# Kernel optimization log

Measured on AMD Instinct MI355X. Metric: run time of the kernel, lower is better.

Reference implementation:

```python
import jax, jax.numpy as jnp
import numpy as np

B, C, H, W = 2, 64, 128, 128
K, SCALE, NUM_RES = 3, 2, 2
KK = K * K


def conv(x, w, b, pad=0):
    y = jax.lax.conv_general_dilated(x, w, (1, 1), [(pad, pad), (pad, pad)],
                                     dimension_numbers=('NCHW', 'OIHW', 'NCHW'))
    return y + b[None, :, None, None]


def unfold_dilated(x, k, d):
    # mimics nn.Unfold(kernel_size=k, dilation=d, padding=(k//2)*d) -> (b, c, k*k, h, w)
    pad = (k // 2) * d
    b, c, h, w = x.shape
    xp = jnp.pad(x, ((0, 0), (0, 0), (pad, pad), (pad, pad)))
    slices = [xp[:, :, i * d:i * d + h, j * d:j * d + w]
              for i in range(k) for j in range(k)]
    return jnp.stack(slices, axis=2)


def setup_inputs() -> dict:
    key = jax.random.key(0)
    ks = jax.random.split(key, 32)
    def p(k, shape, s=0.05):
        return jax.random.normal(k, shape, dtype=jnp.float32) * s
    H2, W2 = H * SCALE, W * SCALE
    return {
        'depth':  p(ks[0], (B, C, H2, W2), 1.0),
        'guide':  p(ks[1], (B, C, H2, W2), 1.0),
        'inputs': p(ks[2], (B, C, H, W), 1.0),
        # depth_kernel branch: 1x1 C->C (ReLU), 1x1 C->k^2
        'dk_w1': p(ks[3], (C, C, 1, 1)), 'dk_b1': jnp.zeros((C,), jnp.float32),
        'dk_w2': p(ks[4], (KK, C, 1, 1)), 'dk_b2': jnp.zeros((KK,), jnp.float32),
        # guide_kernel branch
        'gk_w1': p(ks[5], (C, C, 1, 1)), 'gk_b1': jnp.zeros((C,), jnp.float32),
        'gk_w2': p(ks[6], (KK, C, 1, 1)), 'gk_b2': jnp.zeros((KK,), jnp.float32),
        # weight_net: 3x3 2C->C (ReLU), 3x3 C->C (ReLU, TUnet stand-in), 3x3 C->1
        'wn_w1': p(ks[7], (C, 2 * C, 3, 3)), 'wn_b1': jnp.zeros((C,), jnp.float32),
        'wn_w2': p(ks[8], (C, C, 3, 3)), 'wn_b2': jnp.zeros((C,), jnp.float32),
        'wn_w3': p(ks[9], (1, C, 3, 3)), 'wn_b3': jnp.zeros((1,), jnp.float32),
        # residual blocks on inputs: NUM_RES x (conv3x3-ReLU-conv3x3 + skip)
        'rb_w': p(ks[10], (NUM_RES, 2, C, C, 3, 3)),
        'rb_b': jnp.zeros((NUM_RES, 2, C), jnp.float32),
        'aff_scale': 0.5 * KK * jnp.ones((1,), jnp.float32),
    }


def reference(depth, guide, inputs,
              dk_w1, dk_b1, dk_w2, dk_b2,
              gk_w1, gk_b1, gk_w2, gk_b2,
              wn_w1, wn_b1, wn_w2, wn_b2, wn_w3, wn_b3,
              rb_w, rb_b, aff_scale):
    # weight map
    wm = jax.nn.relu(conv(jnp.concatenate([depth, guide], axis=1), wn_w1, wn_b1, 1))
    wm = jax.nn.relu(conv(wm, wn_w2, wn_b2, 1))
    weight_map = conv(wm, wn_w3, wn_b3, 1)                       # (b,1,h_,w_)
    # per-pixel kernels
    dk = conv(jax.nn.relu(conv(depth, dk_w1, dk_b1)), dk_w2, dk_b2)
    gk = conv(jax.nn.relu(conv(guide, gk_w1, gk_b1)), gk_w2, gk_b2)
    dk = jax.nn.softmax(dk, axis=1)
    gk = jax.nn.softmax(gk, axis=1)
    fuse = weight_map * dk + (1.0 - weight_map) * gk
    fuse = jnp.tanh(fuse) / (aff_scale + 1e-8)
    ksum = jnp.maximum(jnp.sum(jnp.abs(fuse), axis=1, keepdims=True) + 1e-4, 1.0)
    fuse = fuse / ksum                                            # (b,k^2,h_,w_)
    # residual conv stack on low-res inputs
    x = inputs
    for i in range(NUM_RES):
        r = jax.nn.relu(conv(x, rb_w[i, 0], rb_b[i, 0], 1))
        r = conv(r, rb_w[i, 1], rb_b[i, 1], 1)
        x = x + r
    b, c, h, w = x.shape
    up = jax.image.resize(x, (b, c, h * SCALE, w * SCALE), method='bilinear')
    unf = unfold_dilated(up, K, SCALE)                            # (b,c,k^2,h_,w_)
    out = jnp.einsum('bkhw,bckhw->bchw', fuse, unf)
    return out
```

## Files before the change

kernel.cpp:

```cpp
#include <hip/hip_runtime.h>
#include <hip/hip_bf16.h>
#include <math.h>
#include <stdint.h>

#define HW2 (256*256)
#define HW1 (128*128)

typedef __attribute__((ext_vector_type(8))) short short8;
typedef __attribute__((ext_vector_type(4))) float floatx4;

__device__ __forceinline__ float b2f(ushort u) {
    union { unsigned int i; float f; } v; v.i = ((unsigned int)u) << 16; return v.f;
}
__device__ __forceinline__ ushort f2b(float f) {
    __hip_bfloat16 h = __float2bfloat16(f); return *(ushort*)&h;
}
__device__ __forceinline__ float fast_tanh(float x) {
    float cx = fminf(fmaxf(x, -15.f), 15.f);
    float t = __expf(2.f * cx);
    return (t - 1.f) / (t + 1.f);
}
__device__ __forceinline__ void gload_lds16(const void* g, void* l) {
    __builtin_amdgcn_global_load_lds(
        (__attribute__((address_space(1))) void*)(uintptr_t)g,
        (__attribute__((address_space(3))) void*)(unsigned)(uintptr_t)l,
        16, 0, 0);
}

__global__ __launch_bounds__(256)
void repack_all(const float* __restrict__ wn_w1, const float* __restrict__ wn_w2,
                const float* __restrict__ rb_w,
                const float* __restrict__ dk_w1, const float* __restrict__ gk_w1,
                const float* __restrict__ dk_w2, const float* __restrict__ gk_w2,
                const float* __restrict__ wn_w3,
                ushort* __restrict__ wt_wn1, ushort* __restrict__ wt_wn2,
                ushort* __restrict__ wt_rb,
                ushort* __restrict__ w1d, ushort* __restrict__ w1g,
                ushort* __restrict__ w2d, ushort* __restrict__ w2g,
                ushort* __restrict__ wt3) {
    int idx = blockIdx.x * 256 + threadIdx.x;
    int role = blockIdx.y;
    if (role == 0) {
        if (idx >= 73728) return;
        int o = idx / 1152; int rem = idx - o * 1152;
        int ci = rem / 9;   int t = rem - ci * 9;
        wt_wn1[(((size_t)(ci >> 5) * 9 + t) * 64 + o) * 32 + (ci & 31)] = f2b(wn_w1[idx]);
    } else if (role <= 5) {
        if (idx >= 36864) return;
        const float* w = (role == 1) ? wn_w2 : rb_w + (size_t)(role - 2) * 36864;
        ushort* wt     = (role == 1) ? wt_wn2 : wt_rb + (size_t)(role - 2) * 36864;
        int o = idx / 576; int rem = idx - o * 576;
        int ci = rem / 9;  int t = rem - ci * 9;
        wt[(((size_t)(ci >> 5) * 9 + t) * 64 + o) * 32 + (ci & 31)] = f2b(w[idx]);
    } else if (role == 6) {
        if (idx >= 10240) return;
        if (idx < 4096)      w1d[idx] = f2b(dk_w1[idx]);
        else if (idx < 8192) w1g[idx - 4096] = f2b(gk_w1[idx - 4096]);
        else if (idx < 9216) { int i = idx - 8192; w2d[i] = (i >> 6) < 9 ? f2b(dk_w2[i]) : (ushort)0; }
        else                 { int i = idx - 9216; w2g[i] = (i >> 6) < 9 ? f2b(gk_w2[i]) : (ushort)0; }
    } else {
        if (idx >= 9216) return;
        int kc = idx / 512; int rem = idx - kc * 512;
        int n = rem >> 5, c = rem & 31;
        int cc = kc / 9, t = kc - cc * 9;
        wt3[idx] = (n == 0) ? f2b(wn_w3[(cc * 32 + c) * 9 + t]) : (ushort)0;
    }
}

__global__ __launch_bounds__(256)
void to_chunked(const float* __restrict__ in, ushort* __restrict__ outc,
                int H, int W, int Cchunks) {
    int P = W + 2, Q = H + 2;
    int plane_px = P * Q;
    int idx = blockIdx.x * 256 + threadIdx.x;
    if (idx >= plane_px) return;
    int py = idx / P, px = idx - py * P;
    int bc = blockIdx.y;
    int b = bc / Cchunks, cc = bc - b * Cchunks;
    ushort* dst = outc + ((size_t)bc * plane_px + idx) * 32;
    short8* d8 = (short8*)dst;
    if (py == 0 || py == Q - 1 || px == 0 || px == P - 1) {
        short8 z = (short8){0, 0, 0, 0, 0, 0, 0, 0};
        d8[0] = z; d8[1] = z; d8[2] = z; d8[3] = z;
        return;
    }
    int y = py - 1, x = px - 1;
    const float* src = in + ((size_t)b * (Cchunks * 32) + cc * 32) * H * W
                          + (size_t)y * W + x;
    ushort tmp[32];
#pragma unroll
    for (int c = 0; c < 32; ++c)
        tmp[c] = f2b(src[(size_t)c * H * W]);
#pragma unroll
    for (int v = 0; v < 4; ++v) d8[v] = *(short8*)&tmp[v * 8];
}

__global__ __launch_bounds__(256)
void to_chunked_hi4(const float* __restrict__ depth, const float* __restrict__ guide,
                    ushort* __restrict__ outc) {
    int gid = blockIdx.x * 256 + threadIdx.x;
    int g   = gid & 63;
    int y   = (gid >> 6) & 255;
    int pl  = gid >> 14;
    const float* srcb = (pl < 4) ? depth : guide;
    int bc = pl & 3;
    int b = bc >> 1, cc = bc & 1;
    const float* src = srcb + ((size_t)b * 64 + cc * 32) * HW2 + (size_t)y * 256 + g * 4;
    ushort tmp[4][32];
#pragma unroll
    for (int c = 0; c < 32; ++c) {
        floatx4 v = *(const floatx4*)&src[(size_t)c * HW2];
        tmp[0][c] = f2b(v[0]); tmp[1][c] = f2b(v[1]);
        tmp[2][c] = f2b(v[2]); tmp[3][c] = f2b(v[3]);
    }
    ushort* dst = outc + ((size_t)pl * 258 * 258 + (size_t)(y + 1) * 258 + (g * 4 + 1)) * 32;
#pragma unroll
    for (int p = 0; p < 4; ++p) {
        short8* d8 = (short8*)(dst + (size_t)p * 32);
        d8[0] = *(short8*)&tmp[p][0];
        d8[1] = *(short8*)&tmp[p][8];
        d8[2] = *(short8*)&tmp[p][16];
        d8[3] = *(short8*)&tmp[p][24];
    }
}

__global__ __launch_bounds__(256)
void zero_border3(ushort* __restrict__ buf256, ushort* __restrict__ buf128,
                  ushort* __restrict__ bufhi) {
    int region = blockIdx.y;
    int H = (region == 1) ? 128 : 256;
    int P = H + 2, Q = H + 2;
    ushort* buf = (region == 0) ? buf256 : (region == 1) ? buf128 : bufhi;
    int nb = 2 * P + 2 * H;
    int idx = blockIdx.x * 256 + threadIdx.x;
    if (idx >= nb * 8) return;
    int pl = idx / nb, r = idx - pl * nb;
    int py, px;
    if (r < P)          { py = 0;     px = r; }
    else if (r < 2 * P) { py = Q - 1; px = r - P; }
    else { int k = r - 2 * P; py = 1 + (k >> 1); px = (k & 1) ? P - 1 : 0; }
    ushort* dst = buf + ((size_t)pl * P * Q + (size_t)py * P + px) * 32;
    short8 z = (short8){0, 0, 0, 0, 0, 0, 0, 0};
    short8* d8 = (short8*)dst;
    d8[0] = z; d8[1] = z; d8[2] = z; d8[3] = z;
}

template<int NCHUNK, int ROWS, bool RELU, bool HAS_SKIP, bool CONCAT2>
__global__ __launch_bounds__(256, 2)
void conv3x3_reg(const ushort* __restrict__ inA, const ushort* __restrict__ inB,
                 const ushort* __restrict__ wt, const float* __restrict__ bias,
                 const ushort* __restrict__ skip, ushort* __restrict__ outc,
                 int H, int W) {
    const int P = W + 2;
    const size_t plane = (size_t)P * (H + 2) * 32;
    int tid = threadIdx.x;
    int wv = tid >> 6, lane = tid & 63, ml = lane & 15, q = lane >> 4;
    int x0 = blockIdx.x * 16;
    int rowsPerBlock = (blockDim.x >> 6) * ROWS;
    int yb = blockIdx.y * rowsPerBlock + wv * ROWS;
    int b = blockIdx.z;

    floatx4 acc[ROWS][4];
#pragma unroll
    for (int r = 0; r < ROWS; ++r)
#pragma unroll
        for (int n = 0; n < 4; ++n) acc[r][n] = (floatx4){0.f, 0.f, 0.f, 0.f};

    for (int cc = 0; cc < NCHUNK; ++cc) {
        const ushort* base;
        if (CONCAT2) {
            constexpr int HC = NCHUNK / 2;
            if (cc < HC) base = inA + ((size_t)(b * HC + cc)) * plane;
            else         base = inB + ((size_t)(b * HC + cc - HC)) * plane;
        } else {
            base = inA + ((size_t)(b * NCHUNK + cc)) * plane;
        }
        const ushort* wb = wt + (size_t)cc * 18432;
#pragma unroll
        for (int dy = 0; dy < 3; ++dy) {
            short8 afr[3][ROWS], bfr[3][4];
#pragma unroll
            for (int dx = 0; dx < 3; ++dx) {
#pragma unroll
                for (int r = 0; r < ROWS; ++r)
                    afr[dx][r] = *(const short8*)&base[((size_t)(yb + r + dy) * P
                                                       + (x0 + ml + dx)) * 32 + q * 8];
#pragma unroll
                for (int n = 0; n < 4; ++n)
                    bfr[dx][n] = *(const short8*)&wb[(size_t)((dy * 3 + dx) * 64
                                                              + n * 16 + ml) * 32 + q * 8];
            }
#pragma unroll
            for (int dx = 0; dx < 3; ++dx)
#pragma unroll
                for (int r = 0; r < ROWS; ++r)
#pragma unroll
                    for (int n = 0; n < 4; ++n)
                        acc[r][n] = __builtin_amdgcn_mfma_f32_16x16x32_bf16(
                            afr[dx][r], bfr[dx][n], acc[r][n], 0, 0, 0);
        }
    }

#pragma unroll
    for (int r = 0; r < ROWS; ++r) {
        int y = yb + r;
#pragma unroll
        for (int n = 0; n < 4; ++n) {
            int ch = n * 16 + ml;
            int occ = ch >> 5, ocl = ch & 31;
            float bs = bias[ch];
            size_t pbase = ((size_t)(b * 2 + occ)) * plane + ((size_t)(y + 1) * P) * 32 + ocl;
#pragma unroll
            for (int e = 0; e < 4; ++e) {
                int x = x0 + q * 4 + e;
                float v = acc[r][n][e] + bs;
                if (RELU) v = fmaxf(v, 0.f);
                if (HAS_SKIP)
                    v += b2f(skip[((size_t)(b * 2 + occ)) * plane
                                  + ((size_t)(y + 1) * P + (x + 1)) * 32 + ocl]);
                outc[pbase + (size_t)(x + 1) * 32] = f2b(v);
            }
        }
    }
}

__global__ __launch_bounds__(256, 2)
void kernels_fuse_mfma(const ushort* __restrict__ depth_c, const ushort* __restrict__ guide_c,
                       const ushort* __restrict__ bufB,
                       const ushort* __restrict__ wt3, const float* __restrict__ wn_b3,
                       const ushort* __restrict__ w1d, const float* __restrict__ b1d,
                       const ushort* __restrict__ w2d, const float* __restrict__ b2d,
                       const ushort* __restrict__ w1g, const float* __restrict__ b1g,
                       const ushort* __restrict__ w2g, const float* __restrict__ b2g,
                       const float* __restrict__ aff, float* __restrict__ fuse_out) {
    __shared__ __align__(16) ushort stage[12672];
    __shared__ __align__(16) ushort hid[2][4][16 * 72];
    __shared__ float wmv[4][16];

    int tid = threadIdx.x;
    int wv = tid >> 6, lane = tid & 63, ml = lane & 15, q = lane >> 4;
    int p0 = blockIdx.x * 64 + wv * 16;
    int b = p0 >> 16, rem0 = p0 & 65535;
    const size_t plane = (size_t)258 * 258 * 32;

    int rem = rem0 + ml;
    int y = rem >> 8, x = rem & 255;
    size_t poff = ((size_t)(y + 1) * 258 + (x + 1)) * 32;

    int pb  = blockIdx.x * 64;
    int y0  = (pb & 65535) >> 8;
    int x0b = pb & 255;

    short8 afr[2][2];
#pragma unroll
    for (int kc = 0; kc < 2; ++kc) {
        afr[0][kc] = *(const short8*)&depth_c[(size_t)(b * 2 + kc) * plane + poff + q * 8];
        afr[1][kc] = *(const short8*)&guide_c[(size_t)(b * 2 + kc) * plane + poff + q * 8];
    }

    const ushort* bbase = bufB + (size_t)(b * 2) * plane;
#pragma unroll
    for (int i = 0; i < 7; ++i) {
        int wofs = i * 4096 + (wv << 10);
        int ofs  = wofs + (lane << 4);
        if (ofs < 25344) {
            int seg = ofs / 4224;
            int within = ofs - seg * 4224;
            int cc2 = seg / 3, r = seg - cc2 * 3;
            const ushort* gsrc = bbase + (size_t)cc2 * plane
                               + ((size_t)(y0 + r) * 258 + x0b) * 32 + (within >> 1);
            gload_lds16(gsrc, (char*)stage + wofs);
        }
    }
    __syncthreads();

    floatx4 acc[2][4];
#pragma unroll
    for (int br = 0; br < 2; ++br)
#pragma unroll
        for (int nt = 0; nt < 4; ++nt) acc[br][nt] = (floatx4){0.f, 0.f, 0.f, 0.f};
#pragma unroll
    for (int nt = 0; nt < 4; ++nt)
#pragma unroll
        for (int kc = 0; kc < 2; ++kc) {
            short8 bD = *(const short8*)&w1d[(size_t)((nt * 16 + ml) * 64 + kc * 32 + q * 8)];
            short8 bG = *(const short8*)&w1g[(size_t)((nt * 16 + ml) * 64 + kc * 32 + q * 8)];
            acc[0][nt] = __builtin_amdgcn_mfma_f32_16x16x32_bf16(afr[0][kc], bD, acc[0][nt], 0, 0, 0);
            acc[1][nt] = __builtin_amdgcn_mfma_f32_16x16x32_bf16(afr[1][kc], bG, acc[1][nt], 0, 0, 0);
        }

    int colb = (wv << 4) + ml;
    floatx4 dw[4];
#pragma unroll
    for (int u = 0; u < 4; ++u) dw[u] = (floatx4){0.f, 0.f, 0.f, 0.f};
#pragma unroll
    for (int t = 0; t < 9; ++t) {
        int dy2 = t / 3, dx2 = t - 3 * dy2;
        short8 a0 = *(const short8*)&stage[(size_t)(dy2 * 66 + colb + dx2) * 32 + q * 8];
        short8 b3 = *(const short8*)&wt3[(size_t)(t * 512 + ml * 32 + q * 8)];
        dw[t & 3] = __builtin_amdgcn_mfma_f32_16x16x32_bf16(a0, b3, dw[t & 3], 0, 0, 0);
    }
#pragma unroll
    for (int t = 0; t < 9; ++t) {
        int dy2 = t / 3, dx2 = t - 3 * dy2;
        short8 a1 = *(const short8*)&stage[(size_t)((3 + dy2) * 66 + colb + dx2) * 32 + q * 8];
        short8 b3 = *(const short8*)&wt3[(size_t)((9 + t) * 512 + ml * 32 + q * 8)];
        dw[t & 3] = __builtin_amdgcn_mfma_f32_16x16x32_bf16(a1, b3, dw[t & 3], 0, 0, 0);
    }
    floatx4 dwm = (dw[0] + dw[1]) + (dw[2] + dw[3]);
    if (ml == 0) {
#pragma unroll
        for (int e = 0; e < 4; ++e) wmv[wv][q * 4 + e] = dwm[e];
    }

#pragma unroll
    for (int br = 0; br < 2; ++br) {
        const float* b1 = br ? b1g : b1d;
        ushort* h = hid[br][wv];
#pragma unroll
        for (int nt = 0; nt < 4; ++nt) {
            float bs = b1[nt * 16 + ml];
#pragma unroll
            for (int e = 0; e < 4; ++e) {
                float v = acc[br][nt][e] + bs;
                v = fmaxf(v, 0.f);
                h[(q * 4 + e) * 72 + nt * 16 + ml] = f2b(v);
            }
        }
    }

    floatx4 d2[2];
    d2[0] = (floatx4){0.f, 0.f, 0.f, 0.f};
    d2[1] = (floatx4){0.f, 0.f, 0.f, 0.f};
#pragma unroll
    for (int kc = 0; kc < 2; ++kc) {
        short8 a2d = *(const short8*)&w2d[(size_t)(ml * 64 + kc * 32 + q * 8)];
        short8 a2g = *(const short8*)&w2g[(size_t)(ml * 64 + kc * 32 + q * 8)];
        short8 hfd = *(const short8*)&hid[0][wv][ml * 72 + kc * 32 + q * 8];
        short8 hfg = *(const short8*)&hid[1][wv][ml * 72 + kc * 32 + q * 8];
        d2[0] = __builtin_amdgcn_mfma_f32_16x16x32_bf16(a2d, hfd, d2[0], 0, 0, 0);
        d2[1] = __builtin_amdgcn_mfma_f32_16x16x32_bf16(a2g, hfg, d2[1], 0, 0, 0);
    }

    float wm = wmv[wv][ml] + wn_b3[0];

    float sm[2][4];
#pragma unroll
    for (int br = 0; br < 2; ++br) {
        const float* b2 = br ? b2g : b2d;
        float lg[4];
#pragma unroll
        for (int e = 0; e < 4; ++e) {
            int j = q * 4 + e;
            lg[e] = (j < 9) ? (d2[br][e] + b2[j]) : -1e30f;
        }
        float m = fmaxf(fmaxf(lg[0], lg[1]), fmaxf(lg[2], lg[3]));
        m = fmaxf(m, __shfl_xor(m, 16));
        m = fmaxf(m, __shfl_xor(m, 32));
        float s = 0.f;
#pragma unroll
        for (int e = 0; e < 4; ++e) { lg[e] = __expf(lg[e] - m); s += lg[e]; }
        s += __shfl_xor(s, 16);
        s += __shfl_xor(s, 32);
        float inv = 1.f / s;
#pragma unroll
        for (int e = 0; e < 4; ++e) sm[br][e] = lg[e] * inv;
    }

    float inv_av = 1.f / (aff[0] + 1e-8f);
    float f[4];
    float s = 0.f;
#pragma unroll
    for (int e = 0; e < 4; ++e) {
        float v = wm * sm[0][e] + (1.f - wm) * sm[1][e];
        v = fast_tanh(v) * inv_av;
        f[e] = v;
        s += fabsf(v);
    }
    s += __shfl_xor(s, 16);
    s += __shfl_xor(s, 32);
    float ksum = s + 1e-4f;
    if (ksum < 1.f) ksum = 1.f;
    float invk = 1.f / ksum;
#pragma unroll
    for (int e = 0; e < 4; ++e) {
        int j = q * 4 + e;
        if (j < 9)
            fuse_out[((size_t)b * 9 + j) * HW2 + rem0 + ml] = f[e] * invk;
    }
}

__global__ __launch_bounds__(256)
void fuse_apply_up(const float* __restrict__ fuse, const ushort* __restrict__ r2c,
                   float* __restrict__ out) {
    int p = blockIdx.x * 256 + threadIdx.x;
    int pl = blockIdx.y;
    int b = pl >> 1, cc = pl & 1;
    int y = p >> 8, x = p & 255;

    int my = y >> 1, mx = x >> 1;
    float wyA = (y & 1) ? 0.75f : 0.25f;  float wyB = 1.f - wyA;
    float wxA = (x & 1) ? 0.75f : 0.25f;  float wxB = 1.f - wxA;
    int R0y = my + ((y & 1) ? 0 : -1) - 1;
    int R0x = mx + ((x & 1) ? 0 : -1) - 1;

    const float* f = fuse + (size_t)b * 9 * HW2 + p;
    float coef[4][4];
#pragma unroll
    for (int k = 0; k < 4; ++k)
#pragma unroll
        for (int l = 0; l < 4; ++l) coef[k][l] = 0.f;

#pragma unroll
    for (int ty = 0; ty < 3; ++ty) {
        int yp = y + (ty - 1) * 2;
        if (yp < 0 || yp > 255) continue;
#pragma unroll
        for (int tx = 0; tx < 3; ++tx) {
            int xp = x + (tx - 1) * 2;
            if (xp < 0 || xp > 255) continue;
            float fv = f[(size_t)(ty * 3 + tx) * HW2];
            coef[ty][tx]         += fv * wyA * wxA;
            coef[ty][tx + 1]     += fv * wyA * wxB;
            coef[ty + 1][tx]     += fv * wyB * wxA;
            coef[ty + 1][tx + 1] += fv * wyB * wxB;
        }
    }

    const ushort* base = r2c + (size_t)pl * 130 * 130 * 32;
    float acc[32];
#pragma unroll
    for (int c = 0; c < 32; ++c) acc[c] = 0.f;
#pragma unroll
    for (int k = 0; k < 4; ++k) {
        int ry = R0y + k; ry = ry < 0 ? 0 : (ry > 127 ? 127 : ry);
#pragma unroll
        for (int l = 0; l < 4; ++l) {
            int rx = R0x + l; rx = rx < 0 ? 0 : (rx > 127 ? 127 : rx);
            float cf = coef[k][l];
            const ushort* u = base + ((size_t)(ry + 1) * 130 + (rx + 1)) * 32;
#pragma unroll
            for (int c = 0; c < 32; ++c) acc[c] = fmaf(cf, b2f(u[c]), acc[c]);
        }
    }
    float* ob = out + ((size_t)(b * 64 + cc * 32)) * HW2 + p;
#pragma unroll
    for (int c = 0; c < 32; ++c) ob[(size_t)c * HW2] = acc[c];
}

extern "C" void kernel_launch(void* const* d_in, const int* in_sizes, int n_in,
                              void* d_out, int out_size, void* d_ws, size_t ws_size,
                              hipStream_t stream) {
    const float* depth  = (const float*)d_in[0];
    const float* guide  = (const float*)d_in[1];
    const float* inputs = (const float*)d_in[2];
    const float* dk_w1  = (const float*)d_in[3];
    const float* dk_b1  = (const float*)d_in[4];
    const float* dk_w2  = (const float*)d_in[5];
    const float* dk_b2  = (const float*)d_in[6];
    const float* gk_w1  = (const float*)d_in[7];
    const float* gk_b1  = (const float*)d_in[8];
    const float* gk_w2  = (const float*)d_in[9];
    const float* gk_b2  = (const float*)d_in[10];
    const float* wn_w1  = (const float*)d_in[11];
    const float* wn_b1  = (const float*)d_in[12];
    const float* wn_w2  = (const float*)d_in[13];
    const float* wn_b2  = (const float*)d_in[14];
    const float* wn_w3  = (const float*)d_in[15];
    const float* wn_b3  = (const float*)d_in[16];
    const float* rb_w   = (const float*)d_in[17];
    const float* rb_b   = (const float*)d_in[18];
    const float* aff    = (const float*)d_in[19];
    float* out = (float*)d_out;

    float* ws = (float*)d_ws;
    size_t off = 0;
    const size_t CH256 = 4260096;
    const size_t CH128 = 1081600;
    ushort* depth_c = (ushort*)(ws + off); off += CH256;
    ushort* guide_c = (ushort*)(ws + off); off += CH256;
    ushort* bufA    = (ushort*)(ws + off); off += CH256;
    ushort* bufB    = (ushort*)(ws + off); off += CH256;
    ushort* inp_c   = (ushort*)(ws + off); off += CH128;
    ushort* r0      = (ushort*)(ws + off); off += CH128;
    ushort* r1      = (ushort*)(ws + off); off += CH128;
    ushort* r2      = (ushort*)(ws + off); off += CH128;
    float* fuse     = ws + off; off += 1179648;
    ushort* wt_wn1  = (ushort*)(ws + off); off += 36864;
    ushort* wt_wn2  = (ushort*)(ws + off); off += 18432;
    ushort* wt_rb   = (ushort*)(ws + off); off += 73728;
    ushort* w1d_b   = (ushort*)(ws + off); off += 2048;
    ushort* w1g_b   = (ushort*)(ws + off); off += 2048;
    ushort* w2d_b   = (ushort*)(ws + off); off += 512;
    ushort* w2g_b   = (ushort*)(ws + off); off += 512;
    ushort* wt3_b   = (ushort*)(ws + off); off += 4608;

    repack_all<<<dim3(288, 8), 256, 0, stream>>>(
        wn_w1, wn_w2, rb_w, dk_w1, gk_w1, dk_w2, gk_w2, wn_w3,
        wt_wn1, wt_wn2, wt_rb, w1d_b, w1g_b, w2d_b, w2g_b, wt3_b);

    to_chunked_hi4<<<512, 256, 0, stream>>>(depth, guide, depth_c);
    to_chunked<<<dim3(67, 4), 256, 0, stream>>>(inputs, inp_c, 128, 128, 2);

    zero_border3<<<dim3(33, 3), 256, 0, stream>>>(bufA, r0, depth_c);

    conv3x3_reg<4, 4, true, false, true ><<<dim3(16, 16, 2), 256, 0, stream>>>(
        depth_c, guide_c, wt_wn1, wn_b1, nullptr, bufA, 256, 256);
    conv3x3_reg<2, 4, true, false, false><<<dim3(16, 16, 2), 256, 0, stream>>>(
        bufA, nullptr, wt_wn2, wn_b2, nullptr, bufB, 256, 256);

    kernels_fuse_mfma<<<2048, 256, 0, stream>>>(depth_c, guide_c, bufB,
                                                wt3_b, wn_b3,
                                                w1d_b, dk_b1, w2d_b, dk_b2,
                                                w1g_b, gk_b1, w2g_b, gk_b2,
                                                aff, fuse);

    conv3x3_reg<2, 2, true,  false, false><<<dim3(8, 16, 2), 256, 0, stream>>>(
        inp_c, nullptr, wt_rb + 0 * 36864, rb_b + 0 * 64, nullptr, r0, 128, 128);
    conv3x3_reg<2, 2, false, true,  false><<<dim3(8, 16, 2), 256, 0, stream>>>(
        r0, nullptr, wt_rb + 1 * 36864, rb_b + 1 * 64, inp_c, r1, 128, 128);
    conv3x3_reg<2, 2, true,  false, false><<<dim3(8, 16, 2), 256, 0, stream>>>(
        r1, nullptr, wt_rb + 2 * 36864, rb_b + 2 * 64, nullptr, r0, 128, 128);
    conv3x3_reg<2, 2, false, true,  false><<<dim3(8, 16, 2), 256, 0, stream>>>(
        r0, nullptr, wt_rb + 3 * 36864, rb_b + 3 * 64, r1, r2, 128, 128);

    fuse_apply_up<<<dim3(256, 4), 256, 0, stream>>>(fuse, r2, out);
}
```

Before: 327.9 us.

## Merge independent branch kernels into combined launches to cut launch count

The four preprocessing kernels are folded into one prep launch that dispatches on block index. The low-resolution residual conv stages are co-scheduled inside the same launches as the high-resolution weight-net convs and the fuse kernel, using extra grid slices. This cuts kernel launches from eleven to six and lets the small 128x128 convs fill idle compute units alongside the larger work. In exchange, the fused kernels share one launch-bounds/register configuration, and blocks of uneven cost run in the same grid.

```diff
diff --git a/kernel.cpp b/kernel.cpp
--- a/kernel.cpp
+++ b/kernel.cpp
@@ -27,19 +27,20 @@
         16, 0, 0);
 }
 
-__global__ __launch_bounds__(256)
-void repack_all(const float* __restrict__ wn_w1, const float* __restrict__ wn_w2,
-                const float* __restrict__ rb_w,
-                const float* __restrict__ dk_w1, const float* __restrict__ gk_w1,
-                const float* __restrict__ dk_w2, const float* __restrict__ gk_w2,
-                const float* __restrict__ wn_w3,
-                ushort* __restrict__ wt_wn1, ushort* __restrict__ wt_wn2,
-                ushort* __restrict__ wt_rb,
-                ushort* __restrict__ w1d, ushort* __restrict__ w1g,
-                ushort* __restrict__ w2d, ushort* __restrict__ w2g,
-                ushort* __restrict__ wt3) {
-    int idx = blockIdx.x * 256 + threadIdx.x;
-    int role = blockIdx.y;
+
+__device__ __forceinline__
+void repack_body(int gx, int role, int tid,
+                 const float* __restrict__ wn_w1, const float* __restrict__ wn_w2,
+                 const float* __restrict__ rb_w,
+                 const float* __restrict__ dk_w1, const float* __restrict__ gk_w1,
+                 const float* __restrict__ dk_w2, const float* __restrict__ gk_w2,
+                 const float* __restrict__ wn_w3,
+                 ushort* __restrict__ wt_wn1, ushort* __restrict__ wt_wn2,
+                 ushort* __restrict__ wt_rb,
+                 ushort* __restrict__ w1d, ushort* __restrict__ w1g,
+                 ushort* __restrict__ w2d, ushort* __restrict__ w2g,
+                 ushort* __restrict__ wt3) {
+    int idx = gx * 256 + tid;
     if (role == 0) {
         if (idx >= 73728) return;
         int o = idx / 1152; int rem = idx - o * 1152;
@@ -67,15 +68,15 @@
     }
 }
 
-__global__ __launch_bounds__(256)
-void to_chunked(const float* __restrict__ in, ushort* __restrict__ outc,
-                int H, int W, int Cchunks) {
+__device__ __forceinline__
+void to_chunked_body(int gx, int bc, int tid,
+                     const float* __restrict__ in, ushort* __restrict__ outc,
+                     int H, int W, int Cchunks) {
     int P = W + 2, Q = H + 2;
     int plane_px = P * Q;
-    int idx = blockIdx.x * 256 + threadIdx.x;
+    int idx = gx * 256 + tid;
     if (idx >= plane_px) return;
     int py = idx / P, px = idx - py * P;
-    int bc = blockIdx.y;
     int b = bc / Cchunks, cc = bc - b * Cchunks;
     ushort* dst = outc + ((size_t)bc * plane_px + idx) * 32;
     short8* d8 = (short8*)dst;
@@ -95,10 +96,11 @@
     for (int v = 0; v < 4; ++v) d8[v] = *(short8*)&tmp[v * 8];
 }
 
-__global__ __launch_bounds__(256)
-void to_chunked_hi4(const float* __restrict__ depth, const float* __restrict__ guide,
-                    ushort* __restrict__ outc) {
-    int gid = blockIdx.x * 256 + threadIdx.x;
+__device__ __forceinline__
+void hi4_body(int bx, int tid,
+              const float* __restrict__ depth, const float* __restrict__ guide,
+              ushort* __restrict__ outc) {
+    int gid = bx * 256 + tid;
     int g   = gid & 63;
     int y   = (gid >> 6) & 255;
     int pl  = gid >> 14;
@@ -124,15 +126,15 @@
     }
 }
 
-__global__ __launch_bounds__(256)
-void zero_border3(ushort* __restrict__ buf256, ushort* __restrict__ buf128,
-                  ushort* __restrict__ bufhi) {
-    int region = blockIdx.y;
+__device__ __forceinline__
+void zero_body(int gx, int region, int tid,
+               ushort* __restrict__ buf256, ushort* __restrict__ buf128,
+               ushort* __restrict__ bufhi) {
     int H = (region == 1) ? 128 : 256;
     int P = H + 2, Q = H + 2;
     ushort* buf = (region == 0) ? buf256 : (region == 1) ? buf128 : bufhi;
     int nb = 2 * P + 2 * H;
-    int idx = blockIdx.x * 256 + threadIdx.x;
+    int idx = gx * 256 + tid;
     if (idx >= nb * 8) return;
     int pl = idx / nb, r = idx - pl * nb;
     int py, px;
@@ -146,19 +148,16 @@
 }
 
 template<int NCHUNK, int ROWS, bool RELU, bool HAS_SKIP, bool CONCAT2>
-__global__ __launch_bounds__(256, 2)
-void conv3x3_reg(const ushort* __restrict__ inA, const ushort* __restrict__ inB,
-                 const ushort* __restrict__ wt, const float* __restrict__ bias,
-                 const ushort* __restrict__ skip, ushort* __restrict__ outc,
-                 int H, int W) {
+__device__ __forceinline__
+void conv_body(const ushort* __restrict__ inA, const ushort* __restrict__ inB,
+               const ushort* __restrict__ wt, const float* __restrict__ bias,
+               const ushort* __restrict__ skip, ushort* __restrict__ outc,
+               int H, int W, int b, int bx, int by, int tid) {
     const int P = W + 2;
     const size_t plane = (size_t)P * (H + 2) * 32;
-    int tid = threadIdx.x;
     int wv = tid >> 6, lane = tid & 63, ml = lane & 15, q = lane >> 4;
-    int x0 = blockIdx.x * 16;
-    int rowsPerBlock = (blockDim.x >> 6) * ROWS;
-    int yb = blockIdx.y * rowsPerBlock + wv * ROWS;
-    int b = blockIdx.z;
+    int x0 = bx * 16;
+    int yb = by * (4 * ROWS) + wv * ROWS;
 
     floatx4 acc[ROWS][4];
 #pragma unroll
@@ -224,22 +223,104 @@
     }
 }
 
+__global__ __launch_bounds__(256)
+void prep_all(const float* __restrict__ depth, const float* __restrict__ guide,
+              const float* __restrict__ inputs,
+              const float* __restrict__ wn_w1, const float* __restrict__ wn_w2,
+              const float* __restrict__ rb_w,
+              const float* __restrict__ dk_w1, const float* __restrict__ gk_w1,
+              const float* __restrict__ dk_w2, const float* __restrict__ gk_w2,
+              const float* __restrict__ wn_w3,
+              ushort* __restrict__ depth_c, ushort* __restrict__ inp_c,
+              ushort* __restrict__ wt_wn1, ushort* __restrict__ wt_wn2,
+              ushort* __restrict__ wt_rb,
+              ushort* __restrict__ w1d, ushort* __restrict__ w1g,
+              ushort* __restrict__ w2d, ushort* __restrict__ w2g,
+              ushort* __restrict__ wt3,
+              ushort* __restrict__ bufA, ushort* __restrict__ r0) {
+    int bx = blockIdx.x, tid = threadIdx.x;
+    if (bx < 512) {
+        hi4_body(bx, tid, depth, guide, depth_c);
+    } else if (bx < 780) {
+        int v = bx - 512;
+        to_chunked_body(v % 67, v / 67, tid, inputs, inp_c, 128, 128, 2);
+    } else if (bx < 3084) {
+        int v = bx - 780;
+        repack_body(v % 288, v / 288, tid, wn_w1, wn_w2, rb_w, dk_w1, gk_w1,
+                    dk_w2, gk_w2, wn_w3, wt_wn1, wt_wn2, wt_rb,
+                    w1d, w1g, w2d, w2g, wt3);
+    } else {
+        int v = bx - 3084;
+        zero_body(v % 33, v / 33, tid, bufA, r0, depth_c);
+    }
+}
+
 __global__ __launch_bounds__(256, 2)
-void kernels_fuse_mfma(const ushort* __restrict__ depth_c, const ushort* __restrict__ guide_c,
-                       const ushort* __restrict__ bufB,
-                       const ushort* __restrict__ wt3, const float* __restrict__ wn_b3,
-                       const ushort* __restrict__ w1d, const float* __restrict__ b1d,
-                       const ushort* __restrict__ w2d, const float* __restrict__ b2d,
-                       const ushort* __restrict__ w1g, const float* __restrict__ b1g,
-                       const ushort* __restrict__ w2g, const float* __restrict__ b2g,
-                       const float* __restrict__ aff, float* __restrict__ fuse_out) {
+void conv_pairA(const ushort* __restrict__ depth_c, const ushort* __restrict__ guide_c,
+                const ushort* __restrict__ wt_wn1, const float* __restrict__ wn_b1,
+                ushort* __restrict__ bufA,
+                const ushort* __restrict__ inp_c, const ushort* __restrict__ wt_rb0,
+                const float* __restrict__ rb_b0, ushort* __restrict__ r0) {
+    int tid = threadIdx.x;
+    if (blockIdx.z == 0) {
+        int idx = blockIdx.y * 16 + blockIdx.x;
+        int b = idx >> 7, rem = idx & 127;
+        conv_body<2, 2, true, false, false>(inp_c, nullptr, wt_rb0, rb_b0, nullptr,
+                                            r0, 128, 128, b, rem & 7, rem >> 3, tid);
+    } else {
+        conv_body<4, 4, true, false, true>(depth_c, guide_c, wt_wn1, wn_b1, nullptr,
+                                           bufA, 256, 256, blockIdx.z - 1,
+                                           blockIdx.x, blockIdx.y, tid);
+    }
+}
+
+__global__ __launch_bounds__(256, 2)
+void conv_pairB(const ushort* __restrict__ bufA,
+                const ushort* __restrict__ wt_wn2, const float* __restrict__ wn_b2,
+                ushort* __restrict__ bufB,
+                const ushort* __restrict__ r0, const ushort* __restrict__ wt_rb1,
+                const float* __restrict__ rb_b1, const ushort* __restrict__ inp_c,
+                ushort* __restrict__ r1) {
+    int tid = threadIdx.x;
+    if (blockIdx.z == 0) {
+        int idx = blockIdx.y * 16 + blockIdx.x;
+        int b = idx >> 7, rem = idx & 127;
+        conv_body<2, 2, false, true, false>(r0, nullptr, wt_rb1, rb_b1, inp_c,
+                                            r1, 128, 128, b, rem & 7, rem >> 3, tid);
+    } else {
+        conv_body<2, 4, true, false, false>(bufA, nullptr, wt_wn2, wn_b2, nullptr,
+                                            bufB, 256, 256, blockIdx.z - 1,
+                                            blockIdx.x, blockIdx.y, tid);
+    }
+}
+
+__global__ __launch_bounds__(256, 2)
+void fuse_rb2(const ushort* __restrict__ depth_c, const ushort* __restrict__ guide_c,
+              const ushort* __restrict__ bufB,
+              const ushort* __restrict__ wt3, const float* __restrict__ wn_b3,
+              const ushort* __restrict__ w1d, const float* __restrict__ b1d,
+              const ushort* __restrict__ w2d, const float* __restrict__ b2d,
+              const ushort* __restrict__ w1g, const float* __restrict__ b1g,
+              const ushort* __restrict__ w2g, const float* __restrict__ b2g,
+              const float* __restrict__ aff, float* __restrict__ fuse_out,
+              const ushort* __restrict__ r1, const ushort* __restrict__ wt_rb2,
+              const float* __restrict__ rb_b2, ushort* __restrict__ r0) {
+    int tid = threadIdx.x;
+    if (blockIdx.x < 256) {
+        int idx = blockIdx.x;
+        int b = idx >> 7, rem = idx & 127;
+        conv_body<2, 2, true, false, false>(r1, nullptr, wt_rb2, rb_b2, nullptr,
+                                            r0, 128, 128, b, rem & 7, rem >> 3, tid);
+        return;
+    }
+    int bxl = blockIdx.x - 256;
+
     __shared__ __align__(16) ushort stage[12672];
     __shared__ __align__(16) ushort hid[2][4][16 * 72];
     __shared__ float wmv[4][16];
 
-    int tid = threadIdx.x;
     int wv = tid >> 6, lane = tid & 63, ml = lane & 15, q = lane >> 4;
-    int p0 = blockIdx.x * 64 + wv * 16;
+    int p0 = bxl * 64 + wv * 16;
     int b = p0 >> 16, rem0 = p0 & 65535;
     const size_t plane = (size_t)258 * 258 * 32;
 
@@ -247,7 +328,7 @@
     int y = rem >> 8, x = rem & 255;
     size_t poff = ((size_t)(y + 1) * 258 + (x + 1)) * 32;
 
-    int pb  = blockIdx.x * 64;
+    int pb  = bxl * 64;
     int y0  = (pb & 65535) >> 8;
     int x0b = pb & 255;
 
@@ -388,6 +469,15 @@
         if (j < 9)
             fuse_out[((size_t)b * 9 + j) * HW2 + rem0 + ml] = f[e] * invk;
     }
+}
+
+__global__ __launch_bounds__(256, 2)
+void conv_single(const ushort* __restrict__ inA, const ushort* __restrict__ wt,
+                 const float* __restrict__ bias, const ushort* __restrict__ skip,
+                 ushort* __restrict__ outc) {
+    conv_body<2, 2, false, true, false>(inA, nullptr, wt, bias, skip, outc,
+                                        128, 128, blockIdx.z,
+                                        blockIdx.x, blockIdx.y, threadIdx.x);
 }
 
 __global__ __launch_bounds__(256)
@@ -495,34 +585,27 @@
     ushort* w2g_b   = (ushort*)(ws + off); off += 512;
     ushort* wt3_b   = (ushort*)(ws + off); off += 4608;
 
-    repack_all<<<dim3(288, 8), 256, 0, stream>>>(
-        wn_w1, wn_w2, rb_w, dk_w1, gk_w1, dk_w2, gk_w2, wn_w3,
-        wt_wn1, wt_wn2, wt_rb, w1d_b, w1g_b, w2d_b, w2g_b, wt3_b);
-
-    to_chunked_hi4<<<512, 256, 0, stream>>>(depth, guide, depth_c);
-    to_chunked<<<dim3(67, 4), 256, 0, stream>>>(inputs, inp_c, 128, 128, 2);
-
-    zero_border3<<<dim3(33, 3), 256, 0, stream>>>(bufA, r0, depth_c);
-
-    conv3x3_reg<4, 4, true, false, true ><<<dim3(16, 16, 2), 256, 0, stream>>>(
-        depth_c, guide_c, wt_wn1, wn_b1, nullptr, bufA, 256, 256);
-    conv3x3_reg<2, 4, true, false, false><<<dim3(16, 16, 2), 256, 0, stream>>>(
-        bufA, nullptr, wt_wn2, wn_b2, nullptr, bufB, 256, 256);
-
-    kernels_fuse_mfma<<<2048, 256, 0, stream>>>(depth_c, guide_c, bufB,
-                                                wt3_b, wn_b3,
-                                                w1d_b, dk_b1, w2d_b, dk_b2,
-                                                w1g_b, gk_b1, w2g_b, gk_b2,
-                                                aff, fuse);
-
-    conv3x3_reg<2, 2, true,  false, false><<<dim3(8, 16, 2), 256, 0, stream>>>(
-        inp_c, nullptr, wt_rb + 0 * 36864, rb_b + 0 * 64, nullptr, r0, 128, 128);
-    conv3x3_reg<2, 2, false, true,  false><<<dim3(8, 16, 2), 256, 0, stream>>>(
-        r0, nullptr, wt_rb + 1 * 36864, rb_b + 1 * 64, inp_c, r1, 128, 128);
-    conv3x3_reg<2, 2, true,  false, false><<<dim3(8, 16, 2), 256, 0, stream>>>(
-        r1, nullptr, wt_rb + 2 * 36864, rb_b + 2 * 64, nullptr, r0, 128, 128);
-    conv3x3_reg<2, 2, false, true,  false><<<dim3(8, 16, 2), 256, 0, stream>>>(
-        r0, nullptr, wt_rb + 3 * 36864, rb_b + 3 * 64, r1, r2, 128, 128);
+    prep_all<<<3183, 256, 0, stream>>>(
+        depth, guide, inputs, wn_w1, wn_w2, rb_w, dk_w1, gk_w1, dk_w2, gk_w2,
+        wn_w3, depth_c, inp_c, wt_wn1, wt_wn2, wt_rb,
+        w1d_b, w1g_b, w2d_b, w2g_b, wt3_b, bufA, r0);
+
+    conv_pairA<<<dim3(16, 16, 3), 256, 0, stream>>>(
+        depth_c, guide_c, wt_wn1, wn_b1, bufA,
+        inp_c, wt_rb + 0 * 36864, rb_b + 0 * 64, r0);
+
+    conv_pairB<<<dim3(16, 16, 3), 256, 0, stream>>>(
+        bufA, wt_wn2, wn_b2, bufB,
+        r0, wt_rb + 1 * 36864, rb_b + 1 * 64, inp_c, r1);
+
+    fuse_rb2<<<2304, 256, 0, stream>>>(
+        depth_c, guide_c, bufB, wt3_b, wn_b3,
+        w1d_b, dk_b1, w2d_b, dk_b2, w1g_b, gk_b1, w2g_b, gk_b2,
+        aff, fuse,
+        r1, wt_rb + 2 * 36864, rb_b + 2 * 64, r0);
+
+    conv_single<<<dim3(8, 16, 2), 256, 0, stream>>>(
+        r0, wt_rb + 3 * 36864, rb_b + 3 * 64, r1, r2);
 
     fuse_apply_up<<<dim3(256, 4), 256, 0, stream>>>(fuse, r2, out);
 }
```

After: 301.1 us. 8.2% less time.
